# Kernel tuning notes

Measured on AMD Instinct MI355X. Metric: run time of the kernel, lower is better.

## Reference

```python
import jax, jax.numpy as jnp
import numpy as np
from jax import lax

B, H, S, D = 4, 12, 4096, 64
TILE = 128


def setup_inputs() -> dict:
    key = jax.random.key(0)
    kq, kk, kv = jax.random.split(key, 3)
    query = jax.random.normal(kq, (B, H, S, D), dtype=jnp.float32)
    key_t = jax.random.normal(kk, (B, H, S, D), dtype=jnp.float32)
    value = jax.random.normal(kv, (B, H, S, D), dtype=jnp.float32)
    return {"query": query, "key": key_t, "value": value}


def _flash_tiled(query, key, value):
    b, h, s, d = query.shape
    scale = d ** (-0.5)
    nq = s // TILE
    nk = s // TILE
    # q tiles: [b, h, nq, TILE, d]; kv tiles scanned along leading axis
    q = query.reshape(b, h, nq, TILE, d)
    k = key.reshape(b, h, nk, TILE, d).transpose(2, 0, 1, 3, 4)    # [nk,b,h,TILE,d]
    v = value.reshape(b, h, nk, TILE, d).transpose(2, 0, 1, 3, 4)  # [nk,b,h,TILE,d]

    out0 = jnp.zeros((b, h, nq, TILE, d), dtype=query.dtype)
    m0 = jnp.full((b, h, nq, TILE, 1), -jnp.inf, dtype=query.dtype)
    s0 = jnp.zeros((b, h, nq, TILE, 1), dtype=query.dtype)

    def step(carry, kv_tiles):
        out, m, ssum = carry
        k_tile, v_tile = kv_tiles
        # scores: [b,h,nq,TILE_q,TILE_k]
        scores = jnp.einsum('bhntd,bhsd->bhnts', q, k_tile) * scale
        cur_max = jnp.max(scores, axis=-1, keepdims=True)
        new_max = jnp.maximum(m, cur_max)
        old_scale = jnp.exp(m - new_max)
        cur_scale = jnp.exp(cur_max - new_max)  # extra factor, faithful to source
        cur_exp = jnp.exp(scores - new_max)
        out = out * old_scale + cur_scale * jnp.einsum('bhnts,bhsd->bhntd', cur_exp, v_tile)
        ssum = ssum * old_scale + cur_scale * jnp.sum(cur_exp, axis=-1, keepdims=True)
        return (out, new_max, ssum), None

    (out, _, ssum), _ = lax.scan(step, (out0, m0, s0), (k, v))
    return (out / ssum).reshape(b, h, s, d)


def reference(query, key, value):
    return _flash_tiled(query, key, value)
```

## Files before the change

### kernel.cpp

```cpp
#include <hip/hip_runtime.h>
#include <hip/hip_bf16.h>


#define S_LEN 4096
#define HD    64
#define QTILE 128
#define KTILE 128
#define NKT   (S_LEN / KTILE)

#define KSTR  72
#define VSTR  136
#define VT_OFF (128 * KSTR)
#define SMEM_U16 (VT_OFF + HD * VSTR)
#define OSTR  68

typedef __attribute__((ext_vector_type(8))) short bf16x8;
typedef __attribute__((ext_vector_type(4))) short bf16x4;
typedef __attribute__((ext_vector_type(4))) float f32x4;

__device__ __forceinline__ unsigned int pk2(float f0, float f1) {
    unsigned int u0 = __builtin_bit_cast(unsigned int, f0) + 0x8000u;
    unsigned int u1 = __builtin_bit_cast(unsigned int, f1) + 0x8000u;
    return __builtin_amdgcn_perm(u1, u0, 0x07060302u);
}

__global__ __launch_bounds__(256, 3)
void fattn_kernel(const float* __restrict__ Q,
                  const float* __restrict__ K,
                  const float* __restrict__ V,
                  float* __restrict__ O) {
    __shared__ __align__(16) unsigned short smem[SMEM_U16];

    const int t    = threadIdx.x;
    const int wave = t >> 6;
    const int lane = t & 63;
    const int m    = lane & 15;
    const int quad = lane >> 4;

    const int qblk = blockIdx.x;
    const int head = blockIdx.y;
    const size_t hbase = (size_t)head * S_LEN * HD;

    unsigned short* const Kl = smem;
    unsigned short* const Vt = smem + VT_OFF;

    bf16x8 qf[2][2];
    #pragma unroll
    for (int rt = 0; rt < 2; ++rt) {
        const float* qp = Q + hbase +
            (size_t)(qblk * QTILE + wave * 32 + rt * 16 + m) * HD + quad * 8;
        #pragma unroll
        for (int kd = 0; kd < 2; ++kd) {
            float4 a = *(const float4*)(qp + kd * 32);
            float4 b = *(const float4*)(qp + kd * 32 + 4);
            union { unsigned int u[4]; bf16x8 v; } cv;
            cv.u[0] = pk2(a.x * 0.125f, a.y * 0.125f);
            cv.u[1] = pk2(a.z * 0.125f, a.w * 0.125f);
            cv.u[2] = pk2(b.x * 0.125f, b.y * 0.125f);
            cv.u[3] = pk2(b.z * 0.125f, b.w * 0.125f);
            qf[rt][kd] = cv.v;
        }
    }

    f32x4 oacc[4][2];
    float mrow[2] = {-INFINITY, -INFINITY};
    float lrow[2] = {0.f, 0.f};
    #pragma unroll
    for (int dt = 0; dt < 4; ++dt)
        #pragma unroll
        for (int rt = 0; rt < 2; ++rt) oacc[dt][rt] = (f32x4){0.f,0.f,0.f,0.f};

    const int r0k = t >> 3;
    const int c0k = (t & 7) * 8;
    const int chk = ((t & 7) + ((t >> 3) & 7)) & 7;
    const int vkey = t & 127;
    const int vdb  = (t >> 7) * 32;
    unsigned short* const vwp = &Vt[vdb * VSTR + vkey];

    float4 va[4][2];
    {
        const float* vp = V + hbase + (size_t)vkey * HD + vdb;
        #pragma unroll
        for (int i = 0; i < 4; ++i) {
            va[i][0] = *(const float4*)(vp + i * 8);
            va[i][1] = *(const float4*)(vp + i * 8 + 4);
        }
    }

    for (int kt = 0; kt < NKT; ++kt) {
        __syncthreads();

        #pragma unroll
        for (int i = 0; i < 4; ++i) {
            #pragma unroll
            for (int j = 0; j < 8; ++j) {
                float f = ((const float*)&va[i][j >> 2])[j & 3];
                unsigned int u = __builtin_bit_cast(unsigned int, f) + 0x8000u;
                vwp[(i * 8 + j) * VSTR] = (unsigned short)(u >> 16);
            }
        }
        {
            const float* kp = K + hbase + (size_t)(kt * KTILE + r0k) * HD + c0k;
            #pragma unroll
            for (int i = 0; i < 4; ++i) {
                float4 a = *(const float4*)(kp + i * 32 * HD);
                float4 b = *(const float4*)(kp + i * 32 * HD + 4);
                union { unsigned int u[4]; bf16x4 v[2]; } cv;
                cv.u[0] = pk2(a.x, a.y); cv.u[1] = pk2(a.z, a.w);
                cv.u[2] = pk2(b.x, b.y); cv.u[3] = pk2(b.z, b.w);
                *(bf16x8*)&Kl[(r0k + i * 32) * KSTR + chk * 8] =
                    *(bf16x8*)&cv.u[0];
            }
        }
        __syncthreads();

        {
            int nk = (kt + 1 < NKT) ? kt + 1 : 0;
            const float* vp = V + hbase + (size_t)(nk * KTILE + vkey) * HD + vdb;
            #pragma unroll
            for (int i = 0; i < 4; ++i) {
                va[i][0] = *(const float4*)(vp + i * 8);
                va[i][1] = *(const float4*)(vp + i * 8 + 4);
            }
        }

        f32x4 sacc[8][2];
        #pragma unroll
        for (int k8 = 0; k8 < 8; ++k8)
            #pragma unroll
            for (int rt = 0; rt < 2; ++rt) sacc[k8][rt] = (f32x4){0.f,0.f,0.f,0.f};

        #pragma unroll
        for (int kd = 0; kd < 2; ++kd) {
            const int coff = (((kd << 2) + quad + m) & 7) << 3;
            #pragma unroll
            for (int k8 = 0; k8 < 8; ++k8) {
                bf16x8 kf = *(const bf16x8*)&Kl[(k8 * 16 + m) * KSTR + coff];
                sacc[k8][0] = __builtin_amdgcn_mfma_f32_16x16x32_bf16(
                    kf, qf[0][kd], sacc[k8][0], 0, 0, 0);
                sacc[k8][1] = __builtin_amdgcn_mfma_f32_16x16x32_bf16(
                    kf, qf[1][kd], sacc[k8][1], 0, 0, 0);
            }
        }

        unsigned int pkv[8][2][2];
        #pragma unroll
        for (int rt = 0; rt < 2; ++rt) {
            float cm = sacc[0][rt][0];
            #pragma unroll
            for (int k8 = 0; k8 < 8; ++k8)
                #pragma unroll
                for (int r = 0; r < 4; ++r)
                    cm = fmaxf(cm, sacc[k8][rt][r]);
            cm = fmaxf(cm, __shfl_xor(cm, 16, 64));
            cm = fmaxf(cm, __shfl_xor(cm, 32, 64));

            float mo  = mrow[rt];
            float mn  = fmaxf(mo, cm);
            float osc = __expf(mo - mn);
            float bias = cm - mn - mn;
            mrow[rt] = mn;

            #pragma unroll
            for (int dt = 0; dt < 4; ++dt) {
                oacc[dt][rt][0] *= osc; oacc[dt][rt][1] *= osc;
                oacc[dt][rt][2] *= osc; oacc[dt][rt][3] *= osc;
            }

            float rs = 0.f;
            #pragma unroll
            for (int k8 = 0; k8 < 8; ++k8) {
                float p0 = __expf(sacc[k8][rt][0] + bias);
                float p1 = __expf(sacc[k8][rt][1] + bias);
                float p2 = __expf(sacc[k8][rt][2] + bias);
                float p3 = __expf(sacc[k8][rt][3] + bias);
                rs += (p0 + p1) + (p2 + p3);
                pkv[k8][rt][0] = pk2(p0, p1);
                pkv[k8][rt][1] = pk2(p2, p3);
            }
            rs += __shfl_xor(rs, 16, 64);
            rs += __shfl_xor(rs, 32, 64);
            lrow[rt] = lrow[rt] * osc + rs;
        }

        #pragma unroll
        for (int kc = 0; kc < 4; ++kc) {
            bf16x8 pf[2];
            #pragma unroll
            for (int rt = 0; rt < 2; ++rt) {
                union { unsigned int u[4]; bf16x8 v; } cv;
                cv.u[0] = pkv[2 * kc][rt][0];
                cv.u[1] = pkv[2 * kc][rt][1];
                cv.u[2] = pkv[2 * kc + 1][rt][0];
                cv.u[3] = pkv[2 * kc + 1][rt][1];
                pf[rt] = cv.v;
            }
            #pragma unroll
            for (int dt = 0; dt < 4; ++dt) {
                const unsigned short* vp0 =
                    &Vt[(dt * 16 + m) * VSTR + kc * 32 + quad * 4];
                bf16x4 a = *(const bf16x4*)vp0;
                bf16x4 b = *(const bf16x4*)(vp0 + 16);
                bf16x8 vf;
                vf[0]=a[0]; vf[1]=a[1]; vf[2]=a[2]; vf[3]=a[3];
                vf[4]=b[0]; vf[5]=b[1]; vf[6]=b[2]; vf[7]=b[3];
                oacc[dt][0] = __builtin_amdgcn_mfma_f32_16x16x32_bf16(
                    vf, pf[0], oacc[dt][0], 0, 0, 0);
                oacc[dt][1] = __builtin_amdgcn_mfma_f32_16x16x32_bf16(
                    vf, pf[1], oacc[dt][1], 0, 0, 0);
            }
        }
    }

    __syncthreads();
    float* Ol = (float*)smem;
    #pragma unroll
    for (int rt = 0; rt < 2; ++rt) {
        float inv = 1.0f / lrow[rt];
        #pragma unroll
        for (int dt = 0; dt < 4; ++dt)
            #pragma unroll
            for (int r = 0; r < 4; ++r)
                Ol[(wave * 32 + rt * 16 + m) * OSTR + dt * 16 + quad * 4 + r] =
                    oacc[dt][rt][r] * inv;
    }
    __syncthreads();
    const size_t obase = hbase + (size_t)(qblk * QTILE) * HD;
    #pragma unroll
    for (int s = 0; s < 8; ++s) {
        int row = s * 16 + (t >> 4);
        int col = (t & 15) * 4;
        *(float4*)&O[obase + (size_t)row * HD + col] =
            *(const float4*)&Ol[row * OSTR + col];
    }
}

extern "C" void kernel_launch(void* const* d_in, const int* in_sizes, int n_in,
                              void* d_out, int out_size, void* d_ws, size_t ws_size,
                              hipStream_t stream) {
    (void)in_sizes; (void)n_in; (void)d_ws; (void)ws_size; (void)out_size;
    const float* Q = (const float*)d_in[0];
    const float* K = (const float*)d_in[1];
    const float* V = (const float*)d_in[2];
    float* O = (float*)d_out;
    dim3 grid(S_LEN / QTILE, 4 * 12);
    fattn_kernel<<<grid, 256, 0, stream>>>(Q, K, V, O);
}
```

Before: 489.2 us.

## Use exp2 softmax, MFMA row sums, lazy rescale, and packed V transpose stores

Folds log2(e) into the Q scale so the softmax can use the native exp2 instruction. The row sum is computed by an extra MFMA against a ones vector, replacing the shuffle-based reductions. Output rescaling is skipped whenever no row max in the wave increased. The V transpose is rewritten to store packed pairs of bf16 (32-bit writes) instead of single 16-bit writes. P is now truncated to bf16 while inputs use round-to-nearest-even, and the final normalization moves to the store phase using rcp. These add two extra MFMAs per chunk, and the truncation of P introduces a small precision change.

```diff
diff --git a/kernel.cpp b/kernel.cpp
--- a/kernel.cpp
+++ b/kernel.cpp
@@ -6,7 +6,7 @@
 #define HD    64
 #define QTILE 128
 #define KTILE 128
-#define NKT   (S_LEN / KTILE)
+#define NKT   32
 
 #define KSTR  72
 #define VSTR  136
@@ -19,9 +19,30 @@
 typedef __attribute__((ext_vector_type(4))) float f32x4;
 
 __device__ __forceinline__ unsigned int pk2(float f0, float f1) {
-    unsigned int u0 = __builtin_bit_cast(unsigned int, f0) + 0x8000u;
-    unsigned int u1 = __builtin_bit_cast(unsigned int, f1) + 0x8000u;
+    unsigned int u0 = __builtin_bit_cast(unsigned int, f0);
+    unsigned int u1 = __builtin_bit_cast(unsigned int, f1);
+    u0 += 0x7FFFu + ((u0 >> 16) & 1u);
+    u1 += 0x7FFFu + ((u1 >> 16) & 1u);
     return __builtin_amdgcn_perm(u1, u0, 0x07060302u);
+}
+__device__ __forceinline__ unsigned int pkt(float f0, float f1) {
+    return __builtin_amdgcn_perm(__builtin_bit_cast(unsigned int, f1),
+                                 __builtin_bit_cast(unsigned int, f0),
+                                 0x07060302u);
+}
+__device__ __forceinline__ float e2(float x) {
+#if __has_builtin(__builtin_amdgcn_exp2f)
+    return __builtin_amdgcn_exp2f(x);
+#else
+    return __expf(x * 0.6931471805599453f);
+#endif
+}
+__device__ __forceinline__ float rcp(float x) {
+#if __has_builtin(__builtin_amdgcn_rcpf)
+    return __builtin_amdgcn_rcpf(x);
+#else
+    return 1.0f / x;
+#endif
 }
 
 __global__ __launch_bounds__(256, 3)
@@ -54,50 +75,62 @@
             float4 a = *(const float4*)(qp + kd * 32);
             float4 b = *(const float4*)(qp + kd * 32 + 4);
             union { unsigned int u[4]; bf16x8 v; } cv;
-            cv.u[0] = pk2(a.x * 0.125f, a.y * 0.125f);
-            cv.u[1] = pk2(a.z * 0.125f, a.w * 0.125f);
-            cv.u[2] = pk2(b.x * 0.125f, b.y * 0.125f);
-            cv.u[3] = pk2(b.z * 0.125f, b.w * 0.125f);
+            const float s = 0.1803368801111f;
+            cv.u[0] = pk2(a.x * s, a.y * s);
+            cv.u[1] = pk2(a.z * s, a.w * s);
+            cv.u[2] = pk2(b.x * s, b.y * s);
+            cv.u[3] = pk2(b.z * s, b.w * s);
             qf[rt][kd] = cv.v;
         }
     }
 
+    bf16x8 ones;
+    {
+        unsigned int oo = (m == 0) ? 0x3F803F80u : 0u;
+        union { unsigned int u[4]; bf16x8 v; } cv;
+        cv.u[0] = oo; cv.u[1] = oo; cv.u[2] = oo; cv.u[3] = oo;
+        ones = cv.v;
+    }
+
     f32x4 oacc[4][2];
+    f32x4 lacc[2];
     float mrow[2] = {-INFINITY, -INFINITY};
-    float lrow[2] = {0.f, 0.f};
     #pragma unroll
     for (int dt = 0; dt < 4; ++dt)
         #pragma unroll
         for (int rt = 0; rt < 2; ++rt) oacc[dt][rt] = (f32x4){0.f,0.f,0.f,0.f};
+    lacc[0] = (f32x4){0.f,0.f,0.f,0.f};
+    lacc[1] = (f32x4){0.f,0.f,0.f,0.f};
 
     const int r0k = t >> 3;
     const int c0k = (t & 7) * 8;
     const int chk = ((t & 7) + ((t >> 3) & 7)) & 7;
-    const int vkey = t & 127;
-    const int vdb  = (t >> 7) * 32;
-    unsigned short* const vwp = &Vt[vdb * VSTR + vkey];
-
-    float4 va[4][2];
+    const int vp_ = t & 63;
+    const int vd0 = (t >> 6) * 16;
+    unsigned short* const kwb = &Kl[r0k * KSTR + chk * 8];
+    unsigned short* const vwb = &Vt[vd0 * VSTR + 2 * vp_];
+    const unsigned short* const kb0 = &Kl[m * KSTR + (((quad + m) & 7) << 3)];
+    const unsigned short* const kb1 = &Kl[m * KSTR + (((4 + quad + m) & 7) << 3)];
+    const unsigned short* const vrb = &Vt[m * VSTR + quad * 4];
+
+    float4 va[2][4];
     {
-        const float* vp = V + hbase + (size_t)vkey * HD + vdb;
-        #pragma unroll
-        for (int i = 0; i < 4; ++i) {
-            va[i][0] = *(const float4*)(vp + i * 8);
-            va[i][1] = *(const float4*)(vp + i * 8 + 4);
-        }
+        const float* vp = V + hbase + (size_t)(2 * vp_) * HD + vd0;
+        #pragma unroll
+        for (int e = 0; e < 2; ++e)
+            #pragma unroll
+            for (int j = 0; j < 4; ++j)
+                va[e][j] = *(const float4*)(vp + e * HD + j * 4);
     }
 
     for (int kt = 0; kt < NKT; ++kt) {
         __syncthreads();
 
         #pragma unroll
-        for (int i = 0; i < 4; ++i) {
-            #pragma unroll
-            for (int j = 0; j < 8; ++j) {
-                float f = ((const float*)&va[i][j >> 2])[j & 3];
-                unsigned int u = __builtin_bit_cast(unsigned int, f) + 0x8000u;
-                vwp[(i * 8 + j) * VSTR] = (unsigned short)(u >> 16);
-            }
+        for (int d = 0; d < 16; ++d) {
+            float f0 = ((const float*)&va[0][0])[d];
+            float f1 = ((const float*)&va[1][0])[d];
+            *(unsigned int*)(vwb + d * VSTR) = pk2(f0, f1);
         }
         {
             const float* kp = K + hbase + (size_t)(kt * KTILE + r0k) * HD + c0k;
@@ -105,23 +138,22 @@
             for (int i = 0; i < 4; ++i) {
                 float4 a = *(const float4*)(kp + i * 32 * HD);
                 float4 b = *(const float4*)(kp + i * 32 * HD + 4);
-                union { unsigned int u[4]; bf16x4 v[2]; } cv;
+                union { unsigned int u[4]; bf16x8 v; } cv;
                 cv.u[0] = pk2(a.x, a.y); cv.u[1] = pk2(a.z, a.w);
                 cv.u[2] = pk2(b.x, b.y); cv.u[3] = pk2(b.z, b.w);
-                *(bf16x8*)&Kl[(r0k + i * 32) * KSTR + chk * 8] =
-                    *(bf16x8*)&cv.u[0];
+                *(bf16x8*)(kwb + i * 32 * KSTR) = cv.v;
             }
         }
         __syncthreads();
 
         {
             int nk = (kt + 1 < NKT) ? kt + 1 : 0;
-            const float* vp = V + hbase + (size_t)(nk * KTILE + vkey) * HD + vdb;
-            #pragma unroll
-            for (int i = 0; i < 4; ++i) {
-                va[i][0] = *(const float4*)(vp + i * 8);
-                va[i][1] = *(const float4*)(vp + i * 8 + 4);
-            }
+            const float* vp = V + hbase + (size_t)(nk * KTILE + 2 * vp_) * HD + vd0;
+            #pragma unroll
+            for (int e = 0; e < 2; ++e)
+                #pragma unroll
+                for (int j = 0; j < 4; ++j)
+                    va[e][j] = *(const float4*)(vp + e * HD + j * 4);
         }
 
         f32x4 sacc[8][2];
@@ -131,56 +163,57 @@
             for (int rt = 0; rt < 2; ++rt) sacc[k8][rt] = (f32x4){0.f,0.f,0.f,0.f};
 
         #pragma unroll
-        for (int kd = 0; kd < 2; ++kd) {
-            const int coff = (((kd << 2) + quad + m) & 7) << 3;
-            #pragma unroll
-            for (int k8 = 0; k8 < 8; ++k8) {
-                bf16x8 kf = *(const bf16x8*)&Kl[(k8 * 16 + m) * KSTR + coff];
-                sacc[k8][0] = __builtin_amdgcn_mfma_f32_16x16x32_bf16(
-                    kf, qf[0][kd], sacc[k8][0], 0, 0, 0);
-                sacc[k8][1] = __builtin_amdgcn_mfma_f32_16x16x32_bf16(
-                    kf, qf[1][kd], sacc[k8][1], 0, 0, 0);
-            }
+        for (int k8 = 0; k8 < 8; ++k8) {
+            bf16x8 kf0 = *(const bf16x8*)(kb0 + k8 * 16 * KSTR);
+            bf16x8 kf1 = *(const bf16x8*)(kb1 + k8 * 16 * KSTR);
+            sacc[k8][0] = __builtin_amdgcn_mfma_f32_16x16x32_bf16(
+                kf0, qf[0][0], sacc[k8][0], 0, 0, 0);
+            sacc[k8][1] = __builtin_amdgcn_mfma_f32_16x16x32_bf16(
+                kf0, qf[1][0], sacc[k8][1], 0, 0, 0);
+            sacc[k8][0] = __builtin_amdgcn_mfma_f32_16x16x32_bf16(
+                kf1, qf[0][1], sacc[k8][0], 0, 0, 0);
+            sacc[k8][1] = __builtin_amdgcn_mfma_f32_16x16x32_bf16(
+                kf1, qf[1][1], sacc[k8][1], 0, 0, 0);
         }
 
         unsigned int pkv[8][2][2];
         #pragma unroll
         for (int rt = 0; rt < 2; ++rt) {
-            float cm = sacc[0][rt][0];
-            #pragma unroll
-            for (int k8 = 0; k8 < 8; ++k8)
-                #pragma unroll
-                for (int r = 0; r < 4; ++r)
-                    cm = fmaxf(cm, sacc[k8][rt][r]);
+            float cm = fmaxf(fmaxf(sacc[0][rt][0], sacc[0][rt][1]),
+                             fmaxf(sacc[0][rt][2], sacc[0][rt][3]));
+            #pragma unroll
+            for (int k8 = 1; k8 < 8; ++k8) {
+                float a = fmaxf(sacc[k8][rt][0], sacc[k8][rt][1]);
+                float b = fmaxf(sacc[k8][rt][2], sacc[k8][rt][3]);
+                cm = fmaxf(cm, fmaxf(a, b));
+            }
             cm = fmaxf(cm, __shfl_xor(cm, 16, 64));
             cm = fmaxf(cm, __shfl_xor(cm, 32, 64));
 
-            float mo  = mrow[rt];
-            float mn  = fmaxf(mo, cm);
-            float osc = __expf(mo - mn);
+            float mo = mrow[rt];
+            float mn = fmaxf(mo, cm);
             float bias = cm - mn - mn;
             mrow[rt] = mn;
 
-            #pragma unroll
-            for (int dt = 0; dt < 4; ++dt) {
-                oacc[dt][rt][0] *= osc; oacc[dt][rt][1] *= osc;
-                oacc[dt][rt][2] *= osc; oacc[dt][rt][3] *= osc;
-            }
-
-            float rs = 0.f;
+            if (__any(cm > mo)) {
+                float osc = e2(mo - mn);
+                #pragma unroll
+                for (int dt = 0; dt < 4; ++dt) {
+                    oacc[dt][rt][0] *= osc; oacc[dt][rt][1] *= osc;
+                    oacc[dt][rt][2] *= osc; oacc[dt][rt][3] *= osc;
+                }
+                lacc[rt][0] *= osc;
+            }
+
             #pragma unroll
             for (int k8 = 0; k8 < 8; ++k8) {
-                float p0 = __expf(sacc[k8][rt][0] + bias);
-                float p1 = __expf(sacc[k8][rt][1] + bias);
-                float p2 = __expf(sacc[k8][rt][2] + bias);
-                float p3 = __expf(sacc[k8][rt][3] + bias);
-                rs += (p0 + p1) + (p2 + p3);
-                pkv[k8][rt][0] = pk2(p0, p1);
-                pkv[k8][rt][1] = pk2(p2, p3);
-            }
-            rs += __shfl_xor(rs, 16, 64);
-            rs += __shfl_xor(rs, 32, 64);
-            lrow[rt] = lrow[rt] * osc + rs;
+                float p0 = e2(sacc[k8][rt][0] + bias);
+                float p1 = e2(sacc[k8][rt][1] + bias);
+                float p2 = e2(sacc[k8][rt][2] + bias);
+                float p3 = e2(sacc[k8][rt][3] + bias);
+                pkv[k8][rt][0] = pkt(p0, p1);
+                pkv[k8][rt][1] = pkt(p2, p3);
+            }
         }
 
         #pragma unroll
@@ -197,18 +230,18 @@
             }
             #pragma unroll
             for (int dt = 0; dt < 4; ++dt) {
-                const unsigned short* vp0 =
-                    &Vt[(dt * 16 + m) * VSTR + kc * 32 + quad * 4];
-                bf16x4 a = *(const bf16x4*)vp0;
-                bf16x4 b = *(const bf16x4*)(vp0 + 16);
-                bf16x8 vf;
-                vf[0]=a[0]; vf[1]=a[1]; vf[2]=a[2]; vf[3]=a[3];
-                vf[4]=b[0]; vf[5]=b[1]; vf[6]=b[2]; vf[7]=b[3];
+                union { struct { bf16x4 lo, hi; } s; bf16x8 v; } uf;
+                uf.s.lo = *(const bf16x4*)(vrb + dt * 16 * VSTR + kc * 32);
+                uf.s.hi = *(const bf16x4*)(vrb + dt * 16 * VSTR + kc * 32 + 16);
                 oacc[dt][0] = __builtin_amdgcn_mfma_f32_16x16x32_bf16(
-                    vf, pf[0], oacc[dt][0], 0, 0, 0);
+                    uf.v, pf[0], oacc[dt][0], 0, 0, 0);
                 oacc[dt][1] = __builtin_amdgcn_mfma_f32_16x16x32_bf16(
-                    vf, pf[1], oacc[dt][1], 0, 0, 0);
-            }
+                    uf.v, pf[1], oacc[dt][1], 0, 0, 0);
+            }
+            lacc[0] = __builtin_amdgcn_mfma_f32_16x16x32_bf16(
+                ones, pf[0], lacc[0], 0, 0, 0);
+            lacc[1] = __builtin_amdgcn_mfma_f32_16x16x32_bf16(
+                ones, pf[1], lacc[1], 0, 0, 0);
         }
     }
 
@@ -216,13 +249,14 @@
     float* Ol = (float*)smem;
     #pragma unroll
     for (int rt = 0; rt < 2; ++rt) {
-        float inv = 1.0f / lrow[rt];
         #pragma unroll
         for (int dt = 0; dt < 4; ++dt)
             #pragma unroll
             for (int r = 0; r < 4; ++r)
                 Ol[(wave * 32 + rt * 16 + m) * OSTR + dt * 16 + quad * 4 + r] =
-                    oacc[dt][rt][r] * inv;
+                    oacc[dt][rt][r];
+        if (quad == 0)
+            Ol[(wave * 32 + rt * 16 + m) * OSTR + 64] = lacc[rt][0];
     }
     __syncthreads();
     const size_t obase = hbase + (size_t)(qblk * QTILE) * HD;
@@ -230,8 +264,12 @@
     for (int s = 0; s < 8; ++s) {
         int row = s * 16 + (t >> 4);
         int col = (t & 15) * 4;
-        *(float4*)&O[obase + (size_t)row * HD + col] =
-            *(const float4*)&Ol[row * OSTR + col];
+        float inv = rcp(Ol[row * OSTR + 64]);
+        const float* src = &Ol[row * OSTR + col];
+        float4 o;
+        o.x = src[0] * inv; o.y = src[1] * inv;
+        o.z = src[2] * inv; o.w = src[3] * inv;
+        *(float4*)&O[obase + (size_t)row * HD + col] = o;
     }
 }
 
```

After: 564.9 us. 1.15x slower.
